# Kernel tuning notes

Hardware: AMD Instinct MI355X
Metric: run time of the kernel (lower is better)

The kernel has to match this reference:

```python
import jax, jax.numpy as jnp
import numpy as np

N_SUBJECTS = 16
N_LABELS = 8
DENS_TEMP = 0.1  # args.ProtoSim_dens_temp


def setup_inputs() -> dict:
    key = jax.random.key(0)
    k1, k2, k3 = jax.random.split(key, 3)
    B, C, D = 16384, 2, 1024
    X_data = jax.random.normal(k1, (B, C, D), dtype=jnp.float32)
    subject = jax.random.randint(k2, (B,), 0, N_SUBJECTS, dtype=jnp.int64) if jax.config.jax_enable_x64 else jax.random.randint(k2, (B,), 0, N_SUBJECTS).astype(jnp.int32)
    labels = jax.random.randint(k3, (B,), 0, N_LABELS).astype(subject.dtype)
    return {"X_data": X_data, "subject": subject, "labels": labels}


def reference(X_data, subject, labels):
    B, C, D = X_data.shape
    K = N_SUBJECTS * N_LABELS  # all (subject,label) groups assumed present
    # contrast_feature = cat(unbind(X_data, 1), 0) -> [B*C, D]
    feat = X_data.swapaxes(0, 1).reshape(B * C, D)
    sub2 = jnp.tile(subject, C)          # cat((subject, subject))
    lab2 = jnp.tile(labels, C)
    # torch.unique sorts -> group g = subject * N_LABELS + label matches loop order
    gid = sub2 * N_LABELS + lab2
    counts = jax.ops.segment_sum(jnp.ones((B * C,), feat.dtype), gid, num_segments=K)  # (K,)
    centroid = jax.ops.segment_sum(feat, gid, num_segments=K) / counts[:, None]       # (K, D)
    # per-row euclidean distance to own group centroid (torch.cdist to 1 point)
    dist = jnp.linalg.norm(feat - centroid[gid], axis=1)                               # (B*C,)
    mean_sqrt = jax.ops.segment_sum(jnp.sqrt(dist), gid, num_segments=K) / counts
    density = mean_sqrt / jnp.log(counts + 10.0)
    density = jnp.where(counts <= 1.0, density.max(), density)
    density = jnp.clip(density, jnp.quantile(density, 0.1), jnp.quantile(density, 0.9))
    density = DENS_TEMP * density / density.mean()                                     # (K,)
    # masks: positives = same label, different subject
    g_sub = jnp.arange(K) // N_LABELS
    g_lab = jnp.arange(K) % N_LABELS
    subj_mask = (sub2[:, None] != g_sub[None, :]).astype(feat.dtype)  # (B*C, K)
    lab_mask = (lab2[:, None] == g_lab[None, :]).astype(feat.dtype)
    mask = subj_mask * lab_mask
    # every row has N_SUBJECTS-1 positives (all groups present), so no row filtering
    sim = (feat @ centroid.T) / density[None, :]                                        # (B*C, K)
    sim = sim - sim.max(axis=1, keepdims=True)
    pos = sim * mask
    logp = jax.nn.log_softmax(pos, axis=1)
    row_loss = -(mask * logp).sum(axis=1) / mask.sum(axis=1)  # soft-target CE / #pos
    return row_loss.reshape(C, B).mean()
```

## Files before the change

### kernel.cpp

```cpp
#include <hip/hip_runtime.h>
#include <hip/hip_bf16.h>
#include <math.h>

#define NSUB 16
#define NLAB 8
#define KG 128
#define BN 16384
#define DD 1024

typedef float v4f __attribute__((ext_vector_type(4)));
typedef short short8v __attribute__((ext_vector_type(8)));

static __device__ __forceinline__ short f2bf(float f) {
    unsigned u = __builtin_bit_cast(unsigned, f);
    unsigned r = (u + 0x7fffu + ((u >> 16) & 1u)) >> 16;
    return (short)r;
}

static __device__ __forceinline__ short8v pack_bf8(float4 lo, float4 hi) {
    union { short8v s; __hip_bfloat162 h[4]; } u;
    u.h[0] = __float22bfloat162_rn(float2{lo.x, lo.y});
    u.h[1] = __float22bfloat162_rn(float2{lo.z, lo.w});
    u.h[2] = __float22bfloat162_rn(float2{hi.x, hi.y});
    u.h[3] = __float22bfloat162_rn(float2{hi.z, hi.w});
    return u.s;
}

static __device__ __forceinline__ float dot4(float4 v) {
    return v.x * v.x + v.y * v.y + v.z * v.z + v.w * v.w;
}

__global__ __launch_bounds__(1024) void k0_gid(const int* __restrict__ subject,
                                               const int* __restrict__ labels,
                                               int* __restrict__ gid, int* __restrict__ cnt) {
    __shared__ int h[KG];
    int t = threadIdx.x;
    if (t < KG) h[t] = 0;
    __syncthreads();
    int b = blockIdx.x * 1024 + t;
    int g = subject[b] * NLAB + labels[b];
    gid[b] = g;
    atomicAdd(&h[g], 1);
    __syncthreads();
    if (t < KG && h[t]) atomicAdd(&cnt[t], h[t]);
}

__global__ __launch_bounds__(1024) void k0c_scatter(const int* __restrict__ gid,
                                                    const int* __restrict__ cnt,
                                                    int* __restrict__ cursor,
                                                    int* __restrict__ rowlist) {
    __shared__ int cval[KG], coff[KG], lcnt[KG], lbase[KG], lcur[KG];
    int t = threadIdx.x;
    if (t < KG) { cval[t] = cnt[t]; lcnt[t] = 0; lcur[t] = 0; }
    __syncthreads();
    if (t < KG) {
        int o = 0;
        for (int j = 0; j < t; ++j) o += cval[j];
        coff[t] = o;
    }
    int b = blockIdx.x * 1024 + t;
    int g = gid[b];
    atomicAdd(&lcnt[g], 1);
    __syncthreads();
    if (t < KG) lbase[t] = coff[t] + (lcnt[t] ? atomicAdd(&cursor[t], lcnt[t]) : 0);
    __syncthreads();
    rowlist[lbase[g] + atomicAdd(&lcur[g], 1)] = b;
}

__global__ __launch_bounds__(256) void k1_centroid(const float* __restrict__ X,
                                                   const int* __restrict__ rowlist,
                                                   const int* __restrict__ cnt,
                                                   unsigned short* __restrict__ Cbf,
                                                   float* __restrict__ cnorm) {
    int g = blockIdx.x >> 2;
    int dq = blockIdx.x & 3;
    int t = threadIdx.x, d = dq * 256 + t;
    int lane = t & 63, w = t >> 6;
    __shared__ int rows[512];
    __shared__ int sh_no[2];
    __shared__ float wsum[4];
    if (w == 0) {
        int v = 0;
        if (lane < g) v += cnt[lane];
        if (lane + 64 < g) v += cnt[lane + 64];
#pragma unroll
        for (int x = 32; x; x >>= 1) v += __shfl_xor(v, x, 64);
        if (lane == 0) { sh_no[0] = v; sh_no[1] = cnt[g]; }
    }
    __syncthreads();
    int o = sh_no[0], n = min(sh_no[1], 512);
    for (int i = t; i < n; i += 256) rows[i] = rowlist[o + i];
    __syncthreads();
    float acc = 0.f;
    int i = 0;
    for (; i + 8 <= n; i += 8) {
        float v[16];
#pragma unroll
        for (int u = 0; u < 8; ++u) {
            size_t base = (size_t)rows[i + u] * 2048 + d;
            v[2 * u] = X[base];
            v[2 * u + 1] = X[base + 1024];
        }
#pragma unroll
        for (int u = 0; u < 16; ++u) acc += v[u];
    }
    for (; i < n; ++i) {
        size_t base = (size_t)rows[i] * 2048 + d;
        acc += X[base] + X[base + 1024];
    }
    float c = acc / (2.f * (float)n);
    Cbf[(size_t)g * DD + d] = (unsigned short)f2bf(c);
    float s = c * c;
#pragma unroll
    for (int x = 32; x; x >>= 1) s += __shfl_xor(s, x, 64);
    if (lane == 0) wsum[w] = s;
    __syncthreads();
    if (t == 0) atomicAdd(&cnorm[g], wsum[0] + wsum[1] + wsum[2] + wsum[3]);
}

__global__ __launch_bounds__(256) void k5a_dot(const float* __restrict__ X,
                                               const unsigned short* __restrict__ Cbf,
                                               const int* __restrict__ gid,
                                               const float* __restrict__ cnorm,
                                               float* __restrict__ Dot,
                                               float* __restrict__ sqrtsum) {
    __shared__ float h[KG];
    int t = threadIdx.x, lane = t & 63;
    if (t < KG) h[t] = 0.f;
    __syncthreads();
    int gw = blockIdx.x * 4 + (t >> 6);
    int row0 = gw * 32;
    int m = lane & 15, q = lane >> 4;
    int r0 = row0 + m, r1 = row0 + 16 + m;
    const float* a0p = X + (size_t)(r0 & (BN - 1)) * 2048 + (size_t)(r0 >> 14) * 1024 + q * 8;
    const float* a1p = X + (size_t)(r1 & (BN - 1)) * 2048 + (size_t)(r1 >> 14) * 1024 + q * 8;
    const unsigned short* bp = Cbf + (size_t)m * DD + q * 8;

    v4f acc[2][8];
#pragma unroll
    for (int i = 0; i < 2; ++i)
#pragma unroll
        for (int j = 0; j < 8; ++j) acc[i][j] = (v4f){0.f, 0.f, 0.f, 0.f};

    float s0 = 0.f, s1 = 0.f;
    short8v caA0, caA1, caB0, caB1, cbA[8], cbB[8];
    {
        float4 t0l = *(const float4*)(a0p), t0h = *(const float4*)(a0p + 4);
        float4 t1l = *(const float4*)(a1p), t1h = *(const float4*)(a1p + 4);
        s0 += dot4(t0l) + dot4(t0h); s1 += dot4(t1l) + dot4(t1h);
        caA0 = pack_bf8(t0l, t0h); caA1 = pack_bf8(t1l, t1h);
        float4 u0l = *(const float4*)(a0p + 32), u0h = *(const float4*)(a0p + 36);
        float4 u1l = *(const float4*)(a1p + 32), u1h = *(const float4*)(a1p + 36);
        s0 += dot4(u0l) + dot4(u0h); s1 += dot4(u1l) + dot4(u1h);
        caB0 = pack_bf8(u0l, u0h); caB1 = pack_bf8(u1l, u1h);
#pragma unroll
        for (int gt = 0; gt < 8; ++gt) {
            cbA[gt] = *(const short8v*)(bp + gt * 16 * DD);
            cbB[gt] = *(const short8v*)(bp + gt * 16 * DD + 32);
        }
    }
    float4 pA0l = *(const float4*)(a0p + 64), pA0h = *(const float4*)(a0p + 68);
    float4 pA1l = *(const float4*)(a1p + 64), pA1h = *(const float4*)(a1p + 68);
    float4 pB0l = *(const float4*)(a0p + 96), pB0h = *(const float4*)(a0p + 100);
    float4 pB1l = *(const float4*)(a1p + 96), pB1h = *(const float4*)(a1p + 100);

    for (int kc = 0; kc < 32; kc += 2) {
        {
            int kb = (kc + 2 <= 31 ? kc + 2 : 31) * 32;
            short8v nb[8];
#pragma unroll
            for (int gt = 0; gt < 8; ++gt) nb[gt] = *(const short8v*)(bp + gt * 16 * DD + kb);
#pragma unroll
            for (int gt = 0; gt < 8; ++gt) {
                acc[0][gt] = __builtin_amdgcn_mfma_f32_16x16x32_bf16(caA0, cbA[gt], acc[0][gt], 0, 0, 0);
                acc[1][gt] = __builtin_amdgcn_mfma_f32_16x16x32_bf16(caA1, cbA[gt], acc[1][gt], 0, 0, 0);
            }
            if (kc < 30) {
                s0 += dot4(pA0l) + dot4(pA0h); s1 += dot4(pA1l) + dot4(pA1h);
                caA0 = pack_bf8(pA0l, pA0h); caA1 = pack_bf8(pA1l, pA1h);
                int kf = (kc + 4 <= 31 ? kc + 4 : 0) * 32;
                pA0l = *(const float4*)(a0p + kf); pA0h = *(const float4*)(a0p + kf + 4);
                pA1l = *(const float4*)(a1p + kf); pA1h = *(const float4*)(a1p + kf + 4);
            }
#pragma unroll
            for (int gt = 0; gt < 8; ++gt) cbA[gt] = nb[gt];
        }
        {
            int kb = (kc + 3 <= 31 ? kc + 3 : 31) * 32;
            short8v nb[8];
#pragma unroll
            for (int gt = 0; gt < 8; ++gt) nb[gt] = *(const short8v*)(bp + gt * 16 * DD + kb);
#pragma unroll
            for (int gt = 0; gt < 8; ++gt) {
                acc[0][gt] = __builtin_amdgcn_mfma_f32_16x16x32_bf16(caB0, cbB[gt], acc[0][gt], 0, 0, 0);
                acc[1][gt] = __builtin_amdgcn_mfma_f32_16x16x32_bf16(caB1, cbB[gt], acc[1][gt], 0, 0, 0);
            }
            if (kc < 30) {
                s0 += dot4(pB0l) + dot4(pB0h); s1 += dot4(pB1l) + dot4(pB1h);
                caB0 = pack_bf8(pB0l, pB0h); caB1 = pack_bf8(pB1l, pB1h);
                int kf = (kc + 5 <= 31 ? kc + 5 : 0) * 32;
                pB0l = *(const float4*)(a0p + kf); pB0h = *(const float4*)(a0p + kf + 4);
                pB1l = *(const float4*)(a1p + kf); pB1h = *(const float4*)(a1p + kf + 4);
            }
#pragma unroll
            for (int gt = 0; gt < 8; ++gt) cbB[gt] = nb[gt];
        }
    }

    s0 += __shfl_xor(s0, 16, 64); s0 += __shfl_xor(s0, 32, 64);
    s1 += __shfl_xor(s1, 16, 64); s1 += __shfl_xor(s1, 32, 64);

#pragma unroll
    for (int tile = 0; tile < 2; ++tile)
#pragma unroll
        for (int reg = 0; reg < 4; ++reg) {
            int row = row0 + tile * 16 + q * 4 + reg;
            int b = row & (BN - 1);
            int g = gid[b];
            float own = 0.f;
#pragma unroll
            for (int gt = 0; gt < 8; ++gt) {
                float v = acc[tile][gt][reg];
                Dot[(size_t)row * KG + gt * 16 + m] = v;
                if ((g >> 4) == gt) own = v;
            }
            float rn = __shfl(tile ? s1 : s0, q * 4 + reg, 64);
            if ((g & 15) == m) {
                float d2 = fmaxf(rn - 2.f * own + cnorm[g], 0.f);
                atomicAdd(&h[g], sqrtf(sqrtf(d2)));
            }
        }
    __syncthreads();
    if (t < KG && h[t] != 0.f) atomicAdd(&sqrtsum[t], h[t]);
}

__global__ __launch_bounds__(256) void k5b_loss(const float* __restrict__ Dot,
                                                const int* __restrict__ gid,
                                                const float* __restrict__ sqrtsum,
                                                const int* __restrict__ cnt,
                                                float* __restrict__ out) {
    __shared__ float tmp[KG], d1s[KG], qv[4];
    __shared__ float recipDen[KG];
    __shared__ float wsum[4];
    int t = threadIdx.x;
    float cntf = 0.f, d0 = 0.f, v = 0.f;
    if (t < KG) {
        cntf = 2.f * (float)cnt[t];
        d0 = (sqrtsum[t] / cntf) / logf(cntf + 10.f);
        tmp[t] = d0;
    }
    __syncthreads();
    if (t < KG) {
        float dmax = -INFINITY;
        for (int j = 0; j < KG; ++j) dmax = fmaxf(dmax, tmp[j]);
        v = (cntf <= 1.f) ? dmax : d0;
        d1s[t] = v;
    }
    __syncthreads();
    if (t < KG) {
        int less = 0, eq = 0;
        for (int j = 0; j < KG; ++j) {
            float u = d1s[j];
            less += (u < v) ? 1 : 0;
            eq += (u == v) ? 1 : 0;
        }
        const int ppos[4] = {12, 13, 114, 115};
        for (int qq = 0; qq < 4; ++qq)
            if (less <= ppos[qq] && ppos[qq] < less + eq) qv[qq] = v;
    }
    __syncthreads();
    if (t < KG) {
        float q10 = 0.3f * qv[0] + 0.7f * qv[1];
        float q90 = 0.7f * qv[2] + 0.3f * qv[3];
        tmp[t] = fminf(fmaxf(v, q10), q90);
    }
    __syncthreads();
    if (t < KG) {
        float sum = 0.f;
        for (int j = 0; j < KG; ++j) sum += tmp[j];
        float mean = sum / (float)KG;
        recipDen[t] = mean / (0.1f * tmp[t]);
    }
    __syncthreads();
    int row = blockIdx.x * 256 + t;
    int b = row & (BN - 1);
    int g = gid[b];
    int s = g >> 3, l = g & 7;
    int lp = (l >> 2) & 1, lc = l & 3;
    const float4* dp = (const float4*)(Dot + (size_t)row * KG);
    float mx = -INFINITY;
    float psave[16];
#pragma unroll
    for (int c = 0; c < 32; ++c) {
        float4 dv = dp[c];
        float4 rv = *(const float4*)&recipDen[c * 4];
        float x0 = dv.x * rv.x, x1 = dv.y * rv.y, x2 = dv.z * rv.z, x3 = dv.w * rv.w;
        mx = fmaxf(mx, fmaxf(fmaxf(x0, x1), fmaxf(x2, x3)));
        if ((c & 1) == lp) {
            float sel = (lc == 0) ? x0 : (lc == 1) ? x1 : (lc == 2) ? x2 : x3;
            psave[c >> 1] = sel;
        }
    }
    float S = 0.f, P = 0.f;
#pragma unroll
    for (int j = 0; j < 16; ++j) {
        float pv = psave[j] - mx;
        float e = expf(pv);
        bool use = (j != s);
        S += use ? e : 0.f;
        P += use ? pv : 0.f;
    }
    float ll = logf(113.f + S) - P * (1.f / 15.f);
#pragma unroll
    for (int x = 32; x; x >>= 1) ll += __shfl_xor(ll, x, 64);
    int lane = t & 63, w = t >> 6;
    if (lane == 0) wsum[w] = ll;
    __syncthreads();
    if (t == 0) atomicAdd(out, (wsum[0] + wsum[1] + wsum[2] + wsum[3]) * (1.f / 32768.f));
}

extern "C" void kernel_launch(void* const* d_in, const int* in_sizes, int n_in,
                              void* d_out, int out_size, void* d_ws, size_t ws_size,
                              hipStream_t stream) {
    const float* X = (const float*)d_in[0];
    const int* subject = (const int*)d_in[1];
    const int* labels = (const int*)d_in[2];
    float* out = (float*)d_out;
    char* w = (char*)d_ws;
    int* gid = (int*)(w + 0);
    int* cnt = (int*)(w + 65536);
    float* sqrtsum = (float*)(w + 66048);
    float* cnorm = (float*)(w + 66560);
    int* cursor = (int*)(w + 67072);
    int* rowlist = (int*)(w + 131072);
    unsigned short* Cbf = (unsigned short*)(w + 262144);
    float* Dot = (float*)(w + 2097152);

    hipMemsetAsync(w + 65536, 0, 2048, stream);
    hipMemsetAsync(out, 0, sizeof(float), stream);

    k0_gid<<<16, 1024, 0, stream>>>(subject, labels, gid, cnt);
    k0c_scatter<<<16, 1024, 0, stream>>>(gid, cnt, cursor, rowlist);
    k1_centroid<<<KG * 4, 256, 0, stream>>>(X, rowlist, cnt, Cbf, cnorm);
    k5a_dot<<<256, 256, 0, stream>>>(X, Cbf, gid, cnorm, Dot, sqrtsum);
    k5b_loss<<<128, 256, 0, stream>>>(Dot, gid, sqrtsum, cnt, out);
}
```

Baseline: 273.8 us.

## Replace global atomics with per-block partial histograms and sums, widen centroid loads

Global atomic accumulators for counts, centroid norms and sqrt-distance sums are replaced with per-block partial arrays that later kernels reduce deterministically. This drops the workspace memset and the cursor atomics in the scatter step. The centroid kernel now has each thread load float2 pairs with half as many blocks, and its unroll depth is doubled. The goal is less launch and atomic overhead. In exchange, the loss kernel does extra serial reads over 256 partials, and the centroid kernel has fewer blocks in flight.

```diff
diff --git a/kernel.cpp b/kernel.cpp
--- a/kernel.cpp
+++ b/kernel.cpp
@@ -32,7 +32,7 @@
 
 __global__ __launch_bounds__(1024) void k0_gid(const int* __restrict__ subject,
                                                const int* __restrict__ labels,
-                                               int* __restrict__ gid, int* __restrict__ cnt) {
+                                               int* __restrict__ gid, int* __restrict__ hist) {
     __shared__ int h[KG];
     int t = threadIdx.x;
     if (t < KG) h[t] = 0;
@@ -42,40 +42,49 @@
     gid[b] = g;
     atomicAdd(&h[g], 1);
     __syncthreads();
-    if (t < KG && h[t]) atomicAdd(&cnt[t], h[t]);
+    if (t < KG) hist[blockIdx.x * KG + t] = h[t];
 }
 
 __global__ __launch_bounds__(1024) void k0c_scatter(const int* __restrict__ gid,
-                                                    const int* __restrict__ cnt,
-                                                    int* __restrict__ cursor,
+                                                    const int* __restrict__ hist,
+                                                    int* __restrict__ cnt,
                                                     int* __restrict__ rowlist) {
-    __shared__ int cval[KG], coff[KG], lcnt[KG], lbase[KG], lcur[KG];
-    int t = threadIdx.x;
-    if (t < KG) { cval[t] = cnt[t]; lcnt[t] = 0; lcur[t] = 0; }
+    __shared__ int tots[KG], base0[KG], lcur[KG];
+    int t = threadIdx.x, bi = blockIdx.x;
+    if (t < KG) {
+        int tot = 0, pre = 0;
+#pragma unroll
+        for (int j = 0; j < 16; ++j) {
+            int v = hist[j * KG + t];
+            tot += v;
+            if (j < bi) pre += v;
+        }
+        tots[t] = tot;
+        base0[t] = pre;
+        lcur[t] = 0;
+        if (bi == 0) cnt[t] = tot;
+    }
     __syncthreads();
     if (t < KG) {
         int o = 0;
-        for (int j = 0; j < t; ++j) o += cval[j];
-        coff[t] = o;
-    }
-    int b = blockIdx.x * 1024 + t;
+        for (int j = 0; j < t; ++j) o += tots[j];
+        base0[t] += o;
+    }
+    __syncthreads();
+    int b = bi * 1024 + t;
     int g = gid[b];
-    atomicAdd(&lcnt[g], 1);
-    __syncthreads();
-    if (t < KG) lbase[t] = coff[t] + (lcnt[t] ? atomicAdd(&cursor[t], lcnt[t]) : 0);
-    __syncthreads();
-    rowlist[lbase[g] + atomicAdd(&lcur[g], 1)] = b;
+    rowlist[base0[g] + atomicAdd(&lcur[g], 1)] = b;
 }
 
 __global__ __launch_bounds__(256) void k1_centroid(const float* __restrict__ X,
                                                    const int* __restrict__ rowlist,
                                                    const int* __restrict__ cnt,
                                                    unsigned short* __restrict__ Cbf,
-                                                   float* __restrict__ cnorm) {
-    int g = blockIdx.x >> 2;
-    int dq = blockIdx.x & 3;
-    int t = threadIdx.x, d = dq * 256 + t;
-    int lane = t & 63, w = t >> 6;
+                                                   float* __restrict__ cnormPart) {
+    int g = blockIdx.x >> 1;
+    int half = blockIdx.x & 1;
+    int t = threadIdx.x, lane = t & 63, w = t >> 6;
+    int d = half * 512 + t * 2;
     __shared__ int rows[512];
     __shared__ int sh_no[2];
     __shared__ float wsum[4];
@@ -91,42 +100,50 @@
     int o = sh_no[0], n = min(sh_no[1], 512);
     for (int i = t; i < n; i += 256) rows[i] = rowlist[o + i];
     __syncthreads();
-    float acc = 0.f;
+    float ax = 0.f, ay = 0.f;
     int i = 0;
-    for (; i + 8 <= n; i += 8) {
-        float v[16];
-#pragma unroll
-        for (int u = 0; u < 8; ++u) {
+    for (; i + 16 <= n; i += 16) {
+        float2 v[32];
+#pragma unroll
+        for (int u = 0; u < 16; ++u) {
             size_t base = (size_t)rows[i + u] * 2048 + d;
-            v[2 * u] = X[base];
-            v[2 * u + 1] = X[base + 1024];
-        }
-#pragma unroll
-        for (int u = 0; u < 16; ++u) acc += v[u];
+            v[2 * u] = *(const float2*)(X + base);
+            v[2 * u + 1] = *(const float2*)(X + base + 1024);
+        }
+#pragma unroll
+        for (int u = 0; u < 32; ++u) { ax += v[u].x; ay += v[u].y; }
     }
     for (; i < n; ++i) {
         size_t base = (size_t)rows[i] * 2048 + d;
-        acc += X[base] + X[base + 1024];
-    }
-    float c = acc / (2.f * (float)n);
-    Cbf[(size_t)g * DD + d] = (unsigned short)f2bf(c);
-    float s = c * c;
+        float2 v0 = *(const float2*)(X + base);
+        float2 v1 = *(const float2*)(X + base + 1024);
+        ax += v0.x + v1.x; ay += v0.y + v1.y;
+    }
+    float inv = 1.f / (2.f * (float)n);
+    float cx = ax * inv, cy = ay * inv;
+    ushort2 cb = make_ushort2((unsigned short)f2bf(cx), (unsigned short)f2bf(cy));
+    *(ushort2*)(Cbf + (size_t)g * DD + d) = cb;
+    float s = cx * cx + cy * cy;
 #pragma unroll
     for (int x = 32; x; x >>= 1) s += __shfl_xor(s, x, 64);
     if (lane == 0) wsum[w] = s;
     __syncthreads();
-    if (t == 0) atomicAdd(&cnorm[g], wsum[0] + wsum[1] + wsum[2] + wsum[3]);
+    if (t == 0) cnormPart[half * KG + g] = wsum[0] + wsum[1] + wsum[2] + wsum[3];
 }
 
 __global__ __launch_bounds__(256) void k5a_dot(const float* __restrict__ X,
                                                const unsigned short* __restrict__ Cbf,
                                                const int* __restrict__ gid,
-                                               const float* __restrict__ cnorm,
+                                               const float* __restrict__ cnormPart,
                                                float* __restrict__ Dot,
-                                               float* __restrict__ sqrtsum) {
+                                               float* __restrict__ sqsPart) {
     __shared__ float h[KG];
+    __shared__ float cnormS[KG];
     int t = threadIdx.x, lane = t & 63;
-    if (t < KG) h[t] = 0.f;
+    if (t < KG) {
+        h[t] = 0.f;
+        cnormS[t] = cnormPart[t] + cnormPart[KG + t];
+    }
     __syncthreads();
     int gw = blockIdx.x * 4 + (t >> 6);
     int row0 = gw * 32;
@@ -226,17 +243,17 @@
             }
             float rn = __shfl(tile ? s1 : s0, q * 4 + reg, 64);
             if ((g & 15) == m) {
-                float d2 = fmaxf(rn - 2.f * own + cnorm[g], 0.f);
+                float d2 = fmaxf(rn - 2.f * own + cnormS[g], 0.f);
                 atomicAdd(&h[g], sqrtf(sqrtf(d2)));
             }
         }
     __syncthreads();
-    if (t < KG && h[t] != 0.f) atomicAdd(&sqrtsum[t], h[t]);
+    if (t < KG) sqsPart[(size_t)blockIdx.x * KG + t] = h[t];
 }
 
 __global__ __launch_bounds__(256) void k5b_loss(const float* __restrict__ Dot,
                                                 const int* __restrict__ gid,
-                                                const float* __restrict__ sqrtsum,
+                                                const float* __restrict__ sqsPart,
                                                 const int* __restrict__ cnt,
                                                 float* __restrict__ out) {
     __shared__ float tmp[KG], d1s[KG], qv[4];
@@ -245,8 +262,12 @@
     int t = threadIdx.x;
     float cntf = 0.f, d0 = 0.f, v = 0.f;
     if (t < KG) {
+        float ss = 0.f;
+        for (int j = 0; j < 256; j += 4)
+            ss += sqsPart[(size_t)j * KG + t] + sqsPart[(size_t)(j + 1) * KG + t] +
+                  sqsPart[(size_t)(j + 2) * KG + t] + sqsPart[(size_t)(j + 3) * KG + t];
         cntf = 2.f * (float)cnt[t];
-        d0 = (sqrtsum[t] / cntf) / logf(cntf + 10.f);
+        d0 = (ss / cntf) / logf(cntf + 10.f);
         tmp[t] = d0;
     }
     __syncthreads();
@@ -328,20 +349,19 @@
     float* out = (float*)d_out;
     char* w = (char*)d_ws;
     int* gid = (int*)(w + 0);
-    int* cnt = (int*)(w + 65536);
-    float* sqrtsum = (float*)(w + 66048);
-    float* cnorm = (float*)(w + 66560);
-    int* cursor = (int*)(w + 67072);
+    int* hist = (int*)(w + 65536);
+    int* cnt = (int*)(w + 73728);
+    float* cnormPart = (float*)(w + 74240);
     int* rowlist = (int*)(w + 131072);
     unsigned short* Cbf = (unsigned short*)(w + 262144);
+    float* sqsPart = (float*)(w + 524288);
     float* Dot = (float*)(w + 2097152);
 
-    hipMemsetAsync(w + 65536, 0, 2048, stream);
     hipMemsetAsync(out, 0, sizeof(float), stream);
 
-    k0_gid<<<16, 1024, 0, stream>>>(subject, labels, gid, cnt);
-    k0c_scatter<<<16, 1024, 0, stream>>>(gid, cnt, cursor, rowlist);
-    k1_centroid<<<KG * 4, 256, 0, stream>>>(X, rowlist, cnt, Cbf, cnorm);
-    k5a_dot<<<256, 256, 0, stream>>>(X, Cbf, gid, cnorm, Dot, sqrtsum);
-    k5b_loss<<<128, 256, 0, stream>>>(Dot, gid, sqrtsum, cnt, out);
-}
+    k0_gid<<<16, 1024, 0, stream>>>(subject, labels, gid, hist);
+    k0c_scatter<<<16, 1024, 0, stream>>>(gid, hist, cnt, rowlist);
+    k1_centroid<<<KG * 2, 256, 0, stream>>>(X, rowlist, cnt, Cbf, cnormPart);
+    k5a_dot<<<256, 256, 0, stream>>>(X, Cbf, gid, cnormPart, Dot, sqsPart);
+    k5b_loss<<<128, 256, 0, stream>>>(Dot, gid, sqsPart, cnt, out);
+}
```

Result: no change. 270.5 us (-1.2%).
